# Kernel tuning notes

Hardware: AMD Instinct MI355X
Metric: run time of the kernel (lower is better)

Reference implementation:

```python
import jax, jax.numpy as jnp
import numpy as np

B, S, H, NH = 4, 2048, 512, 8  # batch, seq, hidden, heads
D = H // NH                    # head dim = 64


def setup_inputs() -> dict:
    key = jax.random.key(0)
    ks = jax.random.split(key, 12)
    wscale = 1.0 / np.sqrt(H)
    mk = lambda k, sh: jax.random.normal(k, sh, jnp.float32)
    return {
        "q": mk(ks[0], (B, S, H)),
        "k": mk(ks[1], (B, S, H)),
        "v": mk(ks[2], (B, S, H)),
        "k_b": mk(ks[3], (B, S, H)),
        "mask": jax.random.randint(ks[4], (B, S), 0, 2).astype(jnp.int32),
        "Wq": mk(ks[5], (H, H)) * wscale, "bq": jnp.zeros((H,), jnp.float32),
        "Wk": mk(ks[6], (H, H)) * wscale, "bk": jnp.zeros((H,), jnp.float32),
        "Wv": mk(ks[7], (H, H)) * wscale, "bv": jnp.zeros((H,), jnp.float32),
        "Wkb": mk(ks[8], (H, H)) * wscale, "bkb": jnp.zeros((H,), jnp.float32),
        "Wo": mk(ks[9], (H, H)) * wscale, "bo": jnp.zeros((H,), jnp.float32),
    }


def _attn(q, k, v, k_b, mask, Wq, bq, Wk, bk, Wv, bv, Wkb, bkb, Wo, bo):
    b, s, h = q.shape
    proj = lambda x, W, bias: (x @ W + bias).reshape(b, s, NH, D).transpose(0, 2, 1, 3)
    qh = proj(q, Wq, bq)      # [b, nh, s, d]
    kh = proj(k, Wk, bk)
    vh = proj(v, Wv, bv)
    kbh = proj(k_b, Wkb, bkb)
    # q@k^T + q@k_b^T == q@(k+k_b)^T, scaled by sqrt(d)
    corr = jnp.einsum('bhqd,bhkd->bhqk', qh, kh + kbh) / jnp.sqrt(jnp.float32(D))
    # torch mask repeat pattern depends only on key index -> broadcast over q and heads
    corr = jnp.where(mask[:, None, None, :] == 0, jnp.float32(-1e9), corr)
    prob = jax.nn.softmax(corr, axis=-1)  # dropout inactive (eval mode)
    hid = jnp.einsum('bhqk,bhkd->bhqd', prob, vh)
    hid = hid.transpose(0, 2, 1, 3).reshape(b, s, h)
    return hid @ Wo + bo


def reference(q, k, v, k_b, mask, Wq, bq, Wk, bk, Wv, bv, Wkb, bkb, Wo, bo):
    return _attn(q, k, v, k_b, mask, Wq, bq, Wk, bk, Wv, bv, Wkb, bkb, Wo, bo)
```

## Files before the change

kernel.cpp:

```cpp
#include <hip/hip_runtime.h>
#include <hip/hip_bf16.h>
#include <math.h>

#define B_  4
#define S_  2048
#define H_  512
#define NH_ 8
#define D_  64

typedef __attribute__((ext_vector_type(8))) short bf16x8;
typedef __attribute__((ext_vector_type(4))) float f32x4;
typedef __attribute__((ext_vector_type(16))) float f32x16;
#define MFMA16(a, b, c) __builtin_amdgcn_mfma_f32_16x16x32_bf16(a, b, c, 0, 0, 0)
#define MFMA32(a, b, c) __builtin_amdgcn_mfma_f32_32x32x16_bf16(a, b, c, 0, 0, 0)

__device__ __forceinline__ unsigned short f2bf(float f) {
    union { float f; unsigned int i; } x; x.f = f;
    unsigned int i = x.i;
    i += 0x7fffu + ((i >> 16) & 1u);
    return (unsigned short)(i >> 16);
}
__device__ __forceinline__ unsigned int pk2(float lo, float hi) {
    union { __hip_bfloat162 h; unsigned int u; } c;
    c.h = __float22bfloat162_rn(make_float2(lo, hi));
    return c.u;
}
__device__ __forceinline__ void gl_lds16(const void* g, void* l) {
    __builtin_amdgcn_global_load_lds(
        (const __attribute__((address_space(1))) unsigned int*)g,
        (__attribute__((address_space(3))) unsigned int*)l, 16, 0, 0);
}

__global__ __launch_bounds__(256) void prep_w(
    const float* __restrict__ W0, const float* __restrict__ W1,
    const float* __restrict__ W2, const float* __restrict__ W3,
    unsigned short* __restrict__ Wt)
{
    const float* Ws[4] = {W0, W1, W2, W3};
    const float* W = Ws[blockIdx.z];
    unsigned short* Y = Wt + (size_t)blockIdx.z * H_ * H_;
    __shared__ float Tl[64][68];
    const int t = threadIdx.x;
    const int k0 = blockIdx.y * 64, n0 = blockIdx.x * 64;
    #pragma unroll
    for (int i = 0; i < 4; ++i) {
        const int e = (t + 256 * i) * 4;
        const int r = e >> 6, c = e & 63;
        const float4 a = *(const float4*)(W + (size_t)(k0 + r) * H_ + n0 + c);
        Tl[c + 0][r] = a.x; Tl[c + 1][r] = a.y;
        Tl[c + 2][r] = a.z; Tl[c + 3][r] = a.w;
    }
    __syncthreads();
    #pragma unroll
    for (int i = 0; i < 4; ++i) {
        const int e = (t + 256 * i) * 4;
        const int n = e >> 6, c = e & 63;
        uint2 p;
        p.x = pk2(Tl[n][c + 0], Tl[n][c + 1]);
        p.y = pk2(Tl[n][c + 2], Tl[n][c + 3]);
        *(uint2*)(Y + (size_t)(n0 + n) * H_ + k0 + c) = p;
    }
}

__global__ __launch_bounds__(256, 3) void proj_all(
    const float* __restrict__ q,  const float* __restrict__ k,
    const float* __restrict__ v,  const float* __restrict__ k_b,
    const unsigned short* __restrict__ Wt,
    const float* __restrict__ bq, const float* __restrict__ bk,
    const float* __restrict__ bkb,const float* __restrict__ bv,
    unsigned short* __restrict__ Qf, unsigned short* __restrict__ Kf,
    unsigned short* __restrict__ Vf)
{
    __shared__ __align__(16) unsigned short LB[17408];
    unsigned short* As = LB;
    unsigned short* Bs = LB + 8192;

    const int z = blockIdx.z;
    const float *X, *bias, *X2 = nullptr, *bias2 = nullptr;
    const unsigned short *Wa, *Wb = nullptr;
    unsigned short* Y;
    bool VT = false;
    const size_t WSZ = (size_t)H_ * H_;
    if (z == 0)      { X = q; Wa = Wt;           bias = bq; Y = Qf; }
    else if (z == 1) { X = k; Wa = Wt + WSZ;     bias = bk;
                       X2 = k_b; Wb = Wt + 2 * WSZ; bias2 = bkb; Y = Kf; }
    else             { X = v; Wa = Wt + 3 * WSZ; bias = bv; Y = Vf; VT = true; }

    const int t = threadIdx.x;
    const int w = t >> 6, lane = t & 63;
    const int quad = lane >> 4, l15 = lane & 15;
    const int wr = w >> 1, wc = w & 1;
    const int m0 = blockIdx.x * 128, n0 = blockIdx.y * 128;

    const f32x4 zero = {0.f, 0.f, 0.f, 0.f};
    f32x4 acc[4][4];
    #pragma unroll
    for (int i = 0; i < 4; ++i)
        #pragma unroll
        for (int j = 0; j < 4; ++j) acc[i][j] = zero;

    const int npass = (X2 != nullptr) ? 2 : 1;
    for (int pass = 0; pass < npass; ++pass) {
        const float* Xp = pass ? X2 : X;
        const unsigned short* Wp = pass ? Wb : Wa;
        for (int kb0 = 0; kb0 < H_; kb0 += 64) {
            __syncthreads();
            #pragma unroll
            for (int i = 0; i < 4; ++i) {
                const int c = w * 4 + i;
                const int u = c * 64 + lane;
                const int row = u >> 3;
                const int sc  = ((u & 7) ^ (row & 7)) << 3;
                gl_lds16(Wp + (size_t)(n0 + row) * H_ + kb0 + sc, Bs + c * 512);
            }
            float4 av[8];
            #pragma unroll
            for (int i = 0; i < 8; ++i) {
                const int e = (t + 256 * i) * 4;
                av[i] = *(const float4*)(Xp + (size_t)(m0 + (e >> 6)) * H_ + kb0 + (e & 63));
            }
            #pragma unroll
            for (int i = 0; i < 8; ++i) {
                const int e = (t + 256 * i) * 4;
                const int row = e >> 6, kc = e & 63;
                uint2 p; p.x = pk2(av[i].x, av[i].y); p.y = pk2(av[i].z, av[i].w);
                *(uint2*)&As[row * 64 + ((((kc >> 3) ^ (row & 7)) << 3) | (kc & 7))] = p;
            }
            __syncthreads();
            #pragma unroll
            for (int ks = 0; ks < 2; ++ks) {
                bf16x8 af[4], bfr[4];
                #pragma unroll
                for (int i = 0; i < 4; ++i) {
                    const int row = wr * 64 + i * 16 + l15;
                    af[i] = *(const bf16x8*)&As[row * 64 +
                                (((ks * 4 + quad) ^ (row & 7)) << 3)];
                }
                #pragma unroll
                for (int j = 0; j < 4; ++j) {
                    const int nrw = wc * 64 + j * 16 + l15;
                    bfr[j] = *(const bf16x8*)&Bs[nrw * 64 +
                                (((ks * 4 + quad) ^ (nrw & 7)) << 3)];
                }
                #pragma unroll
                for (int i = 0; i < 4; ++i)
                    #pragma unroll
                    for (int j = 0; j < 4; ++j)
                        acc[i][j] = MFMA16(af[i], bfr[j], acc[i][j]);
            }
        }
    }

    const int bb = m0 >> 11, s0 = m0 & (S_ - 1);
    if (!VT) {
        #pragma unroll
        for (int i = 0; i < 4; ++i)
            #pragma unroll
            for (int r = 0; r < 4; ++r) {
                const int s = s0 + wr * 64 + i * 16 + quad * 4 + r;
                #pragma unroll
                for (int j = 0; j < 4; ++j) {
                    const int nn = n0 + wc * 64 + j * 16 + l15;
                    const int h = nn >> 6, d = nn & 63;
                    float val = acc[i][j][r] + bias[nn];
                    if (bias2) val += bias2[nn];
                    Y[(((size_t)bb * NH_ + h) * S_ + s) * D_ + d] = f2bf(val);
                }
            }
    } else {
        __syncthreads();
        #pragma unroll
        for (int i = 0; i < 4; ++i)
            #pragma unroll
            for (int r = 0; r < 4; ++r) {
                const int ml = wr * 64 + i * 16 + quad * 4 + r;
                #pragma unroll
                for (int j = 0; j < 4; ++j) {
                    const int nl = wc * 64 + j * 16 + l15;
                    LB[nl * 136 + ml] = f2bf(acc[i][j][r] + bias[n0 + nl]);
                }
            }
        __syncthreads();
        const int nr = t >> 1, half = t & 1;
        const int nn = n0 + nr, h = nn >> 6, d = nn & 63;
        const size_t vbase = (((size_t)bb * NH_ + h) * D_ + d) * S_ + s0 + half * 64;
        #pragma unroll
        for (int i = 0; i < 16; ++i)
            *(ushort4*)(Y + vbase + i * 4) =
                *(const ushort4*)&LB[nr * 136 + half * 64 + i * 4];
    }
}

__global__ __launch_bounds__(256, 4) void attn_mfma(
    unsigned short* QHd,
    const unsigned short* __restrict__ Kh, const unsigned short* __restrict__ Vt,
    const int* __restrict__ mask)
{
    const int b = blockIdx.z, h = blockIdx.y;
    const int q0 = blockIdx.x * 64;
    const int t = threadIdx.x;
    const int w = t >> 6, lane = t & 63;
    const int hi = lane >> 5, l31 = lane & 31;
    const int qg = w & 1, kh = w >> 1;

    __shared__ __align__(16) unsigned short KsL[2 * 4096];
    __shared__ __align__(16) unsigned short VsL[2 * 4096];
    __shared__ float mskf[S_];

    const size_t head = ((size_t)b * NH_ + h) * S_;
    unsigned short* Qbase = QHd + head * D_;
    const unsigned short* Kbase = Kh + head * D_;
    const unsigned short* Vbase = Vt + head * D_;

    for (int i = t; i < S_; i += 256)
        mskf[i] = (mask[b * S_ + i] == 0) ? -1e9f : 0.f;

    bf16x8 qf[4];
    #pragma unroll
    for (int ks = 0; ks < 4; ++ks)
        qf[ks] = *(const bf16x8*)(
            Qbase + (size_t)(q0 + qg * 32 + l31) * D_ + ks * 16 + hi * 8);

    bf16x8 onesA;
    #pragma unroll
    for (int i = 0; i < 8; ++i) onesA[i] = (short)0x3F80;

    f32x16 O0, O1, O2;
    #pragma unroll
    for (int i = 0; i < 16; ++i) { O0[i] = 0.f; O1[i] = 0.f; O2[i] = 0.f; }
    const float SC2 = 0.125f * 1.44269504089f;

    #define STAGE(kt_) do {                                                        \
        const int bf_ = (kt_) & 1, k0_ = (kt_) * 64;                               \
        _Pragma("unroll")                                                          \
        for (int i_ = 0; i_ < 2; ++i_) {                                           \
            const int c_ = w * 2 + i_;                                             \
            const int u_ = c_ * 64 + lane;                                         \
            const int row_ = u_ >> 3;                                              \
            const int sc_ = ((u_ & 7) ^ (row_ & 7)) << 3;                          \
            gl_lds16(Kbase + (size_t)(k0_ + row_) * D_ + sc_,                      \
                     KsL + bf_ * 4096 + c_ * 512);                                 \
            gl_lds16(Vbase + (size_t)row_ * S_ + k0_ + sc_,                        \
                     VsL + bf_ * 4096 + c_ * 512);                                 \
        }                                                                          \
    } while (0)

    STAGE(0);
    __syncthreads();

    for (int kt = 0; kt < S_ / 64; ++kt) {
        const int bf = kt & 1;
        const int k0 = kt * 64;
        if (kt + 1 < S_ / 64) STAGE(kt + 1);

        f32x16 acc;
        #pragma unroll
        for (int i = 0; i < 16; ++i) acc[i] = 0.f;
        const int krow = kh * 32 + l31;
        const unsigned short* Kb = KsL + bf * 4096 + krow * 64;
        const int rwk = krow & 7;
        __builtin_amdgcn_s_setprio(1);
        #pragma unroll
        for (int ks = 0; ks < 4; ++ks) {
            const bf16x8 kf = *(const bf16x8*)&Kb[(((ks * 2 + hi) ^ rwk) << 3)];
            acc = MFMA32(kf, qf[ks], acc);
        }
        __builtin_amdgcn_s_setprio(0);
        float p[16];
        #pragma unroll
        for (int bq = 0; bq < 4; ++bq) {
            const float4 ms4 = *(const float4*)&mskf[k0 + kh * 32 + bq * 8 + hi * 4];
            p[4 * bq + 0] = __builtin_amdgcn_exp2f(fmaf(acc[4 * bq + 0], SC2, ms4.x));
            p[4 * bq + 1] = __builtin_amdgcn_exp2f(fmaf(acc[4 * bq + 1], SC2, ms4.y));
            p[4 * bq + 2] = __builtin_amdgcn_exp2f(fmaf(acc[4 * bq + 2], SC2, ms4.z));
            p[4 * bq + 3] = __builtin_amdgcn_exp2f(fmaf(acc[4 * bq + 3], SC2, ms4.w));
        }
        unsigned pkv[8];
        #pragma unroll
        for (int bq = 0; bq < 4; ++bq) {
            pkv[2 * bq + 0] = pk2(p[4 * bq + 0], p[4 * bq + 1]);
            pkv[2 * bq + 1] = pk2(p[4 * bq + 2], p[4 * bq + 3]);
        }
        bf16x8 pfrag[2];
        #pragma unroll
        for (int ksl = 0; ksl < 2; ++ksl) {
            unsigned m0 = pkv[4 * ksl + 0], m2 = pkv[4 * ksl + 2];
            asm volatile("v_permlane32_swap_b32 %0, %1" : "+v"(m0), "+v"(m2));
            unsigned m1 = pkv[4 * ksl + 1], m3 = pkv[4 * ksl + 3];
            asm volatile("v_permlane32_swap_b32 %0, %1" : "+v"(m1), "+v"(m3));
            union { unsigned u[4]; bf16x8 v; } pu;
            pu.u[0] = m0; pu.u[1] = m1; pu.u[2] = m2; pu.u[3] = m3;
            pfrag[ksl] = pu.v;
        }
        __builtin_amdgcn_s_setprio(1);
        #pragma unroll
        for (int dblk = 0; dblk < 2; ++dblk) {
            const int vrow = dblk * 32 + l31;
            const unsigned short* Vb = VsL + bf * 4096 + vrow * 64;
            const int rwv = vrow & 7;
            #pragma unroll
            for (int ksl = 0; ksl < 2; ++ksl) {
                const bf16x8 vf =
                    *(const bf16x8*)&Vb[(((kh * 4 + ksl * 2 + hi) ^ rwv) << 3)];
                if (dblk == 0) O0 = MFMA32(vf, pfrag[ksl], O0);
                else           O1 = MFMA32(vf, pfrag[ksl], O1);
            }
        }
        O2 = MFMA32(onesA, pfrag[0], O2);
        O2 = MFMA32(onesA, pfrag[1], O2);
        __builtin_amdgcn_s_setprio(0);
        __syncthreads();
    }
    #undef STAGE

    float lsum = O2[0];

    if (kh == 1) {
        float* R = qg ? (float*)VsL : (float*)KsL;
        #pragma unroll
        for (int i = 0; i < 16; ++i) R[lane * 33 + i]      = O0[i];
        #pragma unroll
        for (int i = 0; i < 16; ++i) R[lane * 33 + 16 + i] = O1[i];
        if (hi == 0) R[2112 + l31] = lsum;
    }
    __syncthreads();
    if (kh == 0) {
        const float* R = qg ? (const float*)VsL : (const float*)KsL;
        #pragma unroll
        for (int i = 0; i < 16; ++i) O0[i] += R[lane * 33 + i];
        #pragma unroll
        for (int i = 0; i < 16; ++i) O1[i] += R[lane * 33 + 16 + i];
        lsum += R[2112 + l31];
        const float inv = 1.f / lsum;

        unsigned short* Orow = Qbase + (size_t)(q0 + qg * 32 + l31) * D_;
        #pragma unroll
        for (int dblk = 0; dblk < 2; ++dblk) {
            #pragma unroll
            for (int bq = 0; bq < 4; ++bq) {
                const float v0 = (dblk ? O1[4 * bq + 0] : O0[4 * bq + 0]) * inv;
                const float v1 = (dblk ? O1[4 * bq + 1] : O0[4 * bq + 1]) * inv;
                const float v2 = (dblk ? O1[4 * bq + 2] : O0[4 * bq + 2]) * inv;
                const float v3 = (dblk ? O1[4 * bq + 3] : O0[4 * bq + 3]) * inv;
                uint2 st; st.x = pk2(v0, v1); st.y = pk2(v2, v3);
                *(uint2*)&Orow[dblk * 32 + bq * 8 + hi * 4] = st;
            }
        }
    }
}

__global__ __launch_bounds__(256) void out_mfma(
    const unsigned short* __restrict__ Hd, const unsigned short* __restrict__ Wot,
    const float* __restrict__ bias, float* __restrict__ Out)
{
    __shared__ __align__(16) unsigned short As2[2][8192];
    __shared__ __align__(16) unsigned short Bs2[2][4096];
    const int t = threadIdx.x;
    const int w = t >> 6, lane = t & 63;
    const int quad = lane >> 4, l15 = lane & 15;
    const int wr = w >> 1, wc = w & 1;
    const int m0 = blockIdx.x * 128, n0 = blockIdx.y * 64;
    const int bb = m0 >> 11, s0 = m0 & (S_ - 1);

    const f32x4 zero = {0.f, 0.f, 0.f, 0.f};
    f32x4 acc[4][2];
    #pragma unroll
    for (int i = 0; i < 4; ++i)
        #pragma unroll
        for (int j = 0; j < 2; ++j) acc[i][j] = zero;

    #define OSTAGE(s_, bfx_) do {                                              \
        const int hk_ = (s_);                                                  \
        const unsigned short* Ab_ = Hd + (((size_t)bb * NH_ + hk_) * S_ + s0)  \
                                    * D_;                                      \
        _Pragma("unroll")                                                      \
        for (int i_ = 0; i_ < 4; ++i_) {                                       \
            const int c_ = w * 4 + i_, u_ = c_ * 64 + lane, row_ = u_ >> 3;    \
            const int sc_ = ((u_ & 7) ^ (row_ & 7)) << 3;                      \
            gl_lds16(Ab_ + (size_t)row_ * D_ + sc_, As2[bfx_] + c_ * 512);     \
        }                                                                      \
        _Pragma("unroll")                                                      \
        for (int i_ = 0; i_ < 2; ++i_) {                                       \
            const int c_ = w * 2 + i_, u_ = c_ * 64 + lane, row_ = u_ >> 3;    \
            const int sc_ = ((u_ & 7) ^ (row_ & 7)) << 3;                      \
            gl_lds16(Wot + (size_t)(n0 + row_) * H_ + hk_ * 64 + sc_,          \
                     Bs2[bfx_] + c_ * 512);                                    \
        }                                                                      \
    } while (0)

    OSTAGE(0, 0);
    __syncthreads();

    for (int s = 0; s < 8; ++s) {
        const int cur = s & 1;
        if (s + 1 < 8) OSTAGE(s + 1, cur ^ 1);
        #pragma unroll
        for (int ks = 0; ks < 2; ++ks) {
            bf16x8 af[4], bfr[2];
            #pragma unroll
            for (int i = 0; i < 4; ++i) {
                const int row = wr * 64 + i * 16 + l15;
                af[i] = *(const bf16x8*)&As2[cur][row * 64 +
                            (((ks * 4 + quad) ^ (row & 7)) << 3)];
            }
            #pragma unroll
            for (int j = 0; j < 2; ++j) {
                const int nrw = wc * 32 + j * 16 + l15;
                bfr[j] = *(const bf16x8*)&Bs2[cur][nrw * 64 +
                            (((ks * 4 + quad) ^ (nrw & 7)) << 3)];
            }
            #pragma unroll
            for (int i = 0; i < 4; ++i)
                #pragma unroll
                for (int j = 0; j < 2; ++j)
                    acc[i][j] = MFMA16(af[i], bfr[j], acc[i][j]);
        }
        __syncthreads();
    }
    #undef OSTAGE

    #pragma unroll
    for (int i = 0; i < 4; ++i)
        #pragma unroll
        for (int r = 0; r < 4; ++r) {
            const int m = m0 + wr * 64 + i * 16 + quad * 4 + r;
            #pragma unroll
            for (int j = 0; j < 2; ++j) {
                const int n = n0 + wc * 32 + j * 16 + l15;
                Out[(size_t)m * H_ + n] = acc[i][j][r] + bias[n];
            }
        }
}

__global__ void fill_kernel(float* __restrict__ out, float val, int n) {
    const int i = blockIdx.x * 256 + threadIdx.x;
    if (i < n) out[i] = val;
}

extern "C" void kernel_launch(void* const* d_in, const int* in_sizes, int n_in,
                              void* d_out, int out_size, void* d_ws, size_t ws_size,
                              hipStream_t stream) {
    const float* q   = (const float*)d_in[0];
    const float* k   = (const float*)d_in[1];
    const float* v   = (const float*)d_in[2];
    const float* k_b = (const float*)d_in[3];
    const int*   msk = (const int*)d_in[4];
    const float* Wq  = (const float*)d_in[5];
    const float* bq  = (const float*)d_in[6];
    const float* Wk  = (const float*)d_in[7];
    const float* bk  = (const float*)d_in[8];
    const float* Wv  = (const float*)d_in[9];
    const float* bv  = (const float*)d_in[10];
    const float* Wkb = (const float*)d_in[11];
    const float* bkb = (const float*)d_in[12];
    const float* Wo  = (const float*)d_in[13];
    const float* bo  = (const float*)d_in[14];
    float* out = (float*)d_out;

    const size_t PER  = (size_t)B_ * NH_ * S_ * D_;
    const size_t NEED = 3 * PER * sizeof(unsigned short);
    if (ws_size < NEED) {
        fill_kernel<<<(out_size + 255) / 256, 256, 0, stream>>>(
            out, (float)((ws_size >> 20) + 2), out_size);
        return;
    }
    unsigned short* wsh = (unsigned short*)d_ws;
    unsigned short* Qf  = wsh;
    unsigned short* Kf  = wsh + PER;
    unsigned short* Vf  = wsh + 2 * PER;

    unsigned short* Wt = (unsigned short*)d_out;

    dim3 gw(8, 8, 4);
    prep_w<<<gw, 256, 0, stream>>>(Wq, Wk, Wkb, Wv, Wt);

    dim3 gp((B_ * S_) / 128, H_ / 128, 3);
    proj_all<<<gp, 256, 0, stream>>>(q, k, v, k_b, Wt, bq, bk, bkb, bv, Qf, Kf, Vf);

    dim3 ga(S_ / 64, NH_, B_);
    attn_mfma<<<ga, 256, 0, stream>>>(Qf, Kf, Vf, msk);

    dim3 gw1(8, 8, 1);
    prep_w<<<gw1, 256, 0, stream>>>(Wo, Wo, Wo, Wo, Kf);

    dim3 go((B_ * S_) / 128, H_ / 64, 1);
    out_mfma<<<go, 256, 0, stream>>>(Qf, Kf, bo, out);
}
```

Measured before the change: 232.1 us.

## Split K-projection blocks into halves and shrink output GEMM tiles

The projection kernel previously gave the combined k+k_b projection one block doing two passes, so those blocks did twice the work of the others. Now z=1 and z=2 each cover 64 of the 128 rows over both passes, which balances per-block work across the grid and raises occupancy hints. The output GEMM tile drops from 128x64 to 64x64 rows, doubling the grid and halving LDS use for more parallelism. The cost is more B-tile reloads of the weights for each output row.

Result: slower. 330.6 us (+42.4%).

```diff
diff --git a/kernel.cpp b/kernel.cpp
--- a/kernel.cpp
+++ b/kernel.cpp
@@ -62,7 +62,7 @@
     }
 }
 
-__global__ __launch_bounds__(256, 3) void proj_all(
+__global__ __launch_bounds__(256, 4) void proj_all(
     const float* __restrict__ q,  const float* __restrict__ k,
     const float* __restrict__ v,  const float* __restrict__ k_b,
     const unsigned short* __restrict__ Wt,
@@ -76,21 +76,28 @@
     unsigned short* Bs = LB + 8192;
 
     const int z = blockIdx.z;
-    const float *X, *bias, *X2 = nullptr, *bias2 = nullptr;
-    const unsigned short *Wa, *Wb = nullptr;
+    const bool KD = (z == 1) || (z == 2);
+    const bool VT = (z == 3);
+    const size_t WSZ = (size_t)H_ * H_;
+
+    const float *X1, *X2p = nullptr, *bias1, *bias2p = nullptr;
+    const unsigned short *W1, *W2p = nullptr;
     unsigned short* Y;
-    bool VT = false;
-    const size_t WSZ = (size_t)H_ * H_;
-    if (z == 0)      { X = q; Wa = Wt;           bias = bq; Y = Qf; }
-    else if (z == 1) { X = k; Wa = Wt + WSZ;     bias = bk;
-                       X2 = k_b; Wb = Wt + 2 * WSZ; bias2 = bkb; Y = Kf; }
-    else             { X = v; Wa = Wt + 3 * WSZ; bias = bv; Y = Vf; VT = true; }
+    if (z == 0)      { X1 = q; W1 = Wt;           bias1 = bq; Y = Qf; }
+    else if (KD)     { X1 = k; W1 = Wt + WSZ;     bias1 = bk;
+                       X2p = k_b; W2p = Wt + 2 * WSZ; bias2p = bkb; Y = Kf; }
+    else             { X1 = v; W1 = Wt + 3 * WSZ; bias1 = bv; Y = Vf; }
 
     const int t = threadIdx.x;
     const int w = t >> 6, lane = t & 63;
     const int quad = lane >> 4, l15 = lane & 15;
     const int wr = w >> 1, wc = w & 1;
-    const int m0 = blockIdx.x * 128, n0 = blockIdx.y * 128;
+    const int rhalf = KD ? 32 : 64;
+    const int RI = KD ? 2 : 4;
+    const int nA = KD ? 4 : 8;
+    const int m0 = blockIdx.x * 128 + (KD ? (z - 1) * 64 : 0);
+    const int n0 = blockIdx.y * 128;
+    const int NS = KD ? 16 : 8;
 
     const f32x4 zero = {0.f, 0.f, 0.f, 0.f};
     f32x4 acc[4][4];
@@ -99,55 +106,57 @@
         #pragma unroll
         for (int j = 0; j < 4; ++j) acc[i][j] = zero;
 
-    const int npass = (X2 != nullptr) ? 2 : 1;
-    for (int pass = 0; pass < npass; ++pass) {
-        const float* Xp = pass ? X2 : X;
-        const unsigned short* Wp = pass ? Wb : Wa;
-        for (int kb0 = 0; kb0 < H_; kb0 += 64) {
-            __syncthreads();
-            #pragma unroll
-            for (int i = 0; i < 4; ++i) {
-                const int c = w * 4 + i;
-                const int u = c * 64 + lane;
-                const int row = u >> 3;
-                const int sc  = ((u & 7) ^ (row & 7)) << 3;
-                gl_lds16(Wp + (size_t)(n0 + row) * H_ + kb0 + sc, Bs + c * 512);
-            }
-            float4 av[8];
-            #pragma unroll
-            for (int i = 0; i < 8; ++i) {
+    for (int s = 0; s < NS; ++s) {
+        const float* Xp = (s >= 8) ? X2p : X1;
+        const unsigned short* Wp = (s >= 8) ? W2p : W1;
+        const int kb0 = (s & 7) * 64;
+        __syncthreads();
+        #pragma unroll
+        for (int i = 0; i < 4; ++i) {
+            const int c = w * 4 + i;
+            const int u = c * 64 + lane;
+            const int row = u >> 3;
+            const int sc  = ((u & 7) ^ (row & 7)) << 3;
+            gl_lds16(Wp + (size_t)(n0 + row) * H_ + kb0 + sc, Bs + c * 512);
+        }
+        float4 av[8];
+        #pragma unroll
+        for (int i = 0; i < 8; ++i)
+            if (i < nA) {
                 const int e = (t + 256 * i) * 4;
                 av[i] = *(const float4*)(Xp + (size_t)(m0 + (e >> 6)) * H_ + kb0 + (e & 63));
             }
-            #pragma unroll
-            for (int i = 0; i < 8; ++i) {
+        #pragma unroll
+        for (int i = 0; i < 8; ++i)
+            if (i < nA) {
                 const int e = (t + 256 * i) * 4;
                 const int row = e >> 6, kc = e & 63;
                 uint2 p; p.x = pk2(av[i].x, av[i].y); p.y = pk2(av[i].z, av[i].w);
                 *(uint2*)&As[row * 64 + ((((kc >> 3) ^ (row & 7)) << 3) | (kc & 7))] = p;
             }
-            __syncthreads();
-            #pragma unroll
-            for (int ks = 0; ks < 2; ++ks) {
-                bf16x8 af[4], bfr[4];
-                #pragma unroll
-                for (int i = 0; i < 4; ++i) {
-                    const int row = wr * 64 + i * 16 + l15;
+        __syncthreads();
+        #pragma unroll
+        for (int ks = 0; ks < 2; ++ks) {
+            bf16x8 af[4], bfr[4];
+            #pragma unroll
+            for (int i = 0; i < 4; ++i)
+                if (i < RI) {
+                    const int row = wr * rhalf + i * 16 + l15;
                     af[i] = *(const bf16x8*)&As[row * 64 +
                                 (((ks * 4 + quad) ^ (row & 7)) << 3)];
                 }
-                #pragma unroll
-                for (int j = 0; j < 4; ++j) {
-                    const int nrw = wc * 64 + j * 16 + l15;
-                    bfr[j] = *(const bf16x8*)&Bs[nrw * 64 +
-                                (((ks * 4 + quad) ^ (nrw & 7)) << 3)];
-                }
-                #pragma unroll
-                for (int i = 0; i < 4; ++i)
+            #pragma unroll
+            for (int j = 0; j < 4; ++j) {
+                const int nrw = wc * 64 + j * 16 + l15;
+                bfr[j] = *(const bf16x8*)&Bs[nrw * 64 +
+                            (((ks * 4 + quad) ^ (nrw & 7)) << 3)];
+            }
+            #pragma unroll
+            for (int i = 0; i < 4; ++i)
+                if (i < RI)
                     #pragma unroll
                     for (int j = 0; j < 4; ++j)
                         acc[i][j] = MFMA16(af[i], bfr[j], acc[i][j]);
-            }
         }
     }
 
@@ -155,18 +164,19 @@
     if (!VT) {
         #pragma unroll
         for (int i = 0; i < 4; ++i)
-            #pragma unroll
-            for (int r = 0; r < 4; ++r) {
-                const int s = s0 + wr * 64 + i * 16 + quad * 4 + r;
+            if (i < RI)
                 #pragma unroll
-                for (int j = 0; j < 4; ++j) {
-                    const int nn = n0 + wc * 64 + j * 16 + l15;
-                    const int h = nn >> 6, d = nn & 63;
-                    float val = acc[i][j][r] + bias[nn];
-                    if (bias2) val += bias2[nn];
-                    Y[(((size_t)bb * NH_ + h) * S_ + s) * D_ + d] = f2bf(val);
+                for (int r = 0; r < 4; ++r) {
+                    const int s = s0 + wr * rhalf + i * 16 + quad * 4 + r;
+                    #pragma unroll
+                    for (int j = 0; j < 4; ++j) {
+                        const int nn = n0 + wc * 64 + j * 16 + l15;
+                        const int h = nn >> 6, d = nn & 63;
+                        float val = acc[i][j][r] + bias1[nn];
+                        if (KD) val += bias2p[nn];
+                        Y[(((size_t)bb * NH_ + h) * S_ + s) * D_ + d] = f2bf(val);
+                    }
                 }
-            }
     } else {
         __syncthreads();
         #pragma unroll
@@ -177,7 +187,7 @@
                 #pragma unroll
                 for (int j = 0; j < 4; ++j) {
                     const int nl = wc * 64 + j * 16 + l15;
-                    LB[nl * 136 + ml] = f2bf(acc[i][j][r] + bias[n0 + nl]);
+                    LB[nl * 136 + ml] = f2bf(acc[i][j][r] + bias1[n0 + nl]);
                 }
             }
         __syncthreads();
@@ -349,23 +359,23 @@
     }
 }
 
-__global__ __launch_bounds__(256) void out_mfma(
+__global__ __launch_bounds__(256, 4) void out_mfma(
     const unsigned short* __restrict__ Hd, const unsigned short* __restrict__ Wot,
     const float* __restrict__ bias, float* __restrict__ Out)
 {
-    __shared__ __align__(16) unsigned short As2[2][8192];
+    __shared__ __align__(16) unsigned short As2[2][4096];
     __shared__ __align__(16) unsigned short Bs2[2][4096];
     const int t = threadIdx.x;
     const int w = t >> 6, lane = t & 63;
     const int quad = lane >> 4, l15 = lane & 15;
     const int wr = w >> 1, wc = w & 1;
-    const int m0 = blockIdx.x * 128, n0 = blockIdx.y * 64;
+    const int m0 = blockIdx.x * 64, n0 = blockIdx.y * 64;
     const int bb = m0 >> 11, s0 = m0 & (S_ - 1);
 
     const f32x4 zero = {0.f, 0.f, 0.f, 0.f};
-    f32x4 acc[4][2];
-    #pragma unroll
-    for (int i = 0; i < 4; ++i)
+    f32x4 acc[2][2];
+    #pragma unroll
+    for (int i = 0; i < 2; ++i)
         #pragma unroll
         for (int j = 0; j < 2; ++j) acc[i][j] = zero;
 
@@ -374,15 +384,10 @@
         const unsigned short* Ab_ = Hd + (((size_t)bb * NH_ + hk_) * S_ + s0)  \
                                     * D_;                                      \
         _Pragma("unroll")                                                      \
-        for (int i_ = 0; i_ < 4; ++i_) {                                       \
-            const int c_ = w * 4 + i_, u_ = c_ * 64 + lane, row_ = u_ >> 3;    \
-            const int sc_ = ((u_ & 7) ^ (row_ & 7)) << 3;                      \
-            gl_lds16(Ab_ + (size_t)row_ * D_ + sc_, As2[bfx_] + c_ * 512);     \
-        }                                                                      \
-        _Pragma("unroll")                                                      \
         for (int i_ = 0; i_ < 2; ++i_) {                                       \
             const int c_ = w * 2 + i_, u_ = c_ * 64 + lane, row_ = u_ >> 3;    \
             const int sc_ = ((u_ & 7) ^ (row_ & 7)) << 3;                      \
+            gl_lds16(Ab_ + (size_t)row_ * D_ + sc_, As2[bfx_] + c_ * 512);     \
             gl_lds16(Wot + (size_t)(n0 + row_) * H_ + hk_ * 64 + sc_,          \
                      Bs2[bfx_] + c_ * 512);                                    \
         }                                                                      \
@@ -396,10 +401,10 @@
         if (s + 1 < 8) OSTAGE(s + 1, cur ^ 1);
         #pragma unroll
         for (int ks = 0; ks < 2; ++ks) {
-            bf16x8 af[4], bfr[2];
-            #pragma unroll
-            for (int i = 0; i < 4; ++i) {
-                const int row = wr * 64 + i * 16 + l15;
+            bf16x8 af[2], bfr[2];
+            #pragma unroll
+            for (int i = 0; i < 2; ++i) {
+                const int row = wr * 32 + i * 16 + l15;
                 af[i] = *(const bf16x8*)&As2[cur][row * 64 +
                             (((ks * 4 + quad) ^ (row & 7)) << 3)];
             }
@@ -410,7 +415,7 @@
                             (((ks * 4 + quad) ^ (nrw & 7)) << 3)];
             }
             #pragma unroll
-            for (int i = 0; i < 4; ++i)
+            for (int i = 0; i < 2; ++i)
                 #pragma unroll
                 for (int j = 0; j < 2; ++j)
                     acc[i][j] = MFMA16(af[i], bfr[j], acc[i][j]);
@@ -420,10 +425,10 @@
     #undef OSTAGE
 
     #pragma unroll
-    for (int i = 0; i < 4; ++i)
+    for (int i = 0; i < 2; ++i)
         #pragma unroll
         for (int r = 0; r < 4; ++r) {
-            const int m = m0 + wr * 64 + i * 16 + quad * 4 + r;
+            const int m = m0 + wr * 32 + i * 16 + quad * 4 + r;
             #pragma unroll
             for (int j = 0; j < 2; ++j) {
                 const int n = n0 + wc * 32 + j * 16 + l15;
@@ -474,7 +479,7 @@
     dim3 gw(8, 8, 4);
     prep_w<<<gw, 256, 0, stream>>>(Wq, Wk, Wkb, Wv, Wt);
 
-    dim3 gp((B_ * S_) / 128, H_ / 128, 3);
+    dim3 gp((B_ * S_) / 128, H_ / 128, 4);
     proj_all<<<gp, 256, 0, stream>>>(q, k, v, k_b, Wt, bq, bk, bkb, bv, Qf, Kf, Vf);
 
     dim3 ga(S_ / 64, NH_, B_);
@@ -483,6 +488,6 @@
     dim3 gw1(8, 8, 1);
     prep_w<<<gw1, 256, 0, stream>>>(Wo, Wo, Wo, Wo, Kf);
 
-    dim3 go((B_ * S_) / 128, H_ / 64, 1);
+    dim3 go((B_ * S_) / 64, H_ / 64, 1);
     out_mfma<<<go, 256, 0, stream>>>(Qf, Kf, bo, out);
 }
```
